# Kernel optimization log

Hardware: AMD Instinct MI355X
Metric: run time of the kernel (lower is better)

The kernel has to match this reference:

```python
import jax, jax.numpy as jnp
import numpy as np

B, S, HID, NH = 4, 2048, 1024, 16
DH = HID // NH  # 64
SCALE = 1.0 / float(np.sqrt(DH))


def _linear_params(key, scale=0.02):
    kw, kb = jax.random.split(key)
    W = jax.random.normal(kw, (HID, HID), dtype=jnp.float32) * scale
    b = jax.random.normal(kb, (HID,), dtype=jnp.float32) * scale
    return W, b


def setup_inputs() -> dict:
    key = jax.random.key(0)
    ks = jax.random.split(key, 9)
    x = jax.random.normal(ks[0], (B, S, HID), dtype=jnp.float32)
    reasoning_mask = jax.random.uniform(ks[1], (B, S, 1, 1), dtype=jnp.float32)
    Wq, bq = _linear_params(ks[2])
    Wk, bk = _linear_params(ks[3])
    Wv, bv = _linear_params(ks[4])
    Wqr, bqr = _linear_params(ks[5])
    Wkr, bkr = _linear_params(ks[6])
    Wo, bo = _linear_params(ks[7])
    return {"x": x, "reasoning_mask": reasoning_mask,
            "Wq": Wq, "bq": bq, "Wk": Wk, "bk": bk, "Wv": Wv, "bv": bv,
            "Wqr": Wqr, "bqr": bqr, "Wkr": Wkr, "bkr": bkr, "Wo": Wo, "bo": bo}


def reference(x, reasoning_mask, Wq, bq, Wk, bk, Wv, bv, Wqr, bqr, Wkr, bkr, Wo, bo):
    # Projections: x @ W + b, then view (B, S, NH, DH)
    def proj(W, b):
        return (jnp.einsum('bsh,hd->bsd', x, W) + b).reshape(B, S, NH, DH)

    q = proj(Wq, bq)
    k = proj(Wk, bk)
    v = proj(Wv, bv)
    q_r = proj(Wqr, bqr)
    k_r = proj(Wkr, bkr)

    # Reasoning-gated blend of standard and reasoning projections
    q = q * (1.0 - reasoning_mask) + q_r * reasoning_mask
    k = k * (1.0 - reasoning_mask) + k_r * reasoning_mask

    # Faithful to source: matmul over the LAST two dims of (B,S,NH,DH),
    # i.e. per-token attention ACROSS HEADS -> scores shape (B,S,NH,NH)
    scores = jnp.einsum('bshd,bsed->bshe', q, k) * SCALE
    attn = jax.nn.softmax(scores, axis=-1)  # dropout is identity at eval
    out = jnp.einsum('bshe,bsed->bshd', attn, v)  # (B,S,NH,DH)

    # Faithful transpose(1,2) + contiguous view to (B, S, HID)
    out = jnp.transpose(out, (0, 2, 1, 3)).reshape(B, -1, HID)
    return jnp.einsum('bsh,hd->bsd', out, Wo) + bo
```

## Files before the change

### kernel.cpp

```cpp
#include <hip/hip_runtime.h>
#include <hip/hip_bf16.h>


typedef __attribute__((ext_vector_type(8))) short short8;
typedef __attribute__((ext_vector_type(4))) short short4v;
typedef __attribute__((ext_vector_type(4))) float f32x4;

#define HID 1024
#define NTOK 8192
#define WT_ELEMS (1024 * 1024)

__device__ __forceinline__ short f2bs(float f) {
  __hip_bfloat16 h = __float2bfloat16(f);
  return *reinterpret_cast<short*>(&h);
}
__device__ __forceinline__ float bs2f(short s) {
  __hip_bfloat16 h;
  *reinterpret_cast<short*>(&h) = s;
  return __bfloat162float(h);
}
__device__ __forceinline__ void gload16(const void* g, void* l) {
  __builtin_amdgcn_global_load_lds(
      (const __attribute__((address_space(1))) void*)g,
      (__attribute__((address_space(3))) void*)l, 16, 0, 0);
}

#define BAR() asm volatile("s_barrier" ::: "memory")
#define VMWAIT(N) asm volatile("s_waitcnt vmcnt(" #N ")" ::: "memory")
#define SCB __builtin_amdgcn_sched_barrier(0)
#define PRIO1 __builtin_amdgcn_s_setprio(1)
#define PRIO0 __builtin_amdgcn_s_setprio(0)
#define MFMA16x16 __builtin_amdgcn_mfma_f32_16x16x32_bf16

__global__ __launch_bounds__(256) void prep_kernel(
    const float* __restrict__ W0, const float* __restrict__ W1,
    const float* __restrict__ W2, const float* __restrict__ W3,
    const float* __restrict__ W4, const float* __restrict__ W5,
    const float* __restrict__ X, short* __restrict__ WT, short* __restrict__ XB)
{
  __shared__ short sT[64][68];
  const int bid = blockIdx.x, tid = threadIdx.x;
  if (bid < 1536) {
    const int z = bid >> 8, rem = bid & 255;
    const float* W = z == 0 ? W0 : z == 1 ? W1 : z == 2 ? W2 : z == 3 ? W3
                   : z == 4 ? W4 : W5;
    short* OUT = WT + (size_t)z * WT_ELEMS;
    const int k0 = (rem & 15) * 64, n0 = (rem >> 4) * 64;
    #pragma unroll
    for (int i = 0; i < 4; i++) {
      const int li = tid + i * 256;
      const int kr = li >> 4, c4 = (li & 15) << 2;
      const f32x4 wv = *reinterpret_cast<const f32x4*>(&W[(size_t)(k0 + kr) * HID + n0 + c4]);
      short4v s4;
      #pragma unroll
      for (int j = 0; j < 4; j++) s4[j] = f2bs(wv[j]);
      *reinterpret_cast<short4v*>(&sT[kr][c4]) = s4;
    }
    __syncthreads();
    #pragma unroll
    for (int i = 0; i < 4; i++) {
      const int li = tid + i * 256;
      const int nr = li >> 4, k4 = (li & 15) << 2;
      short4v o;
      #pragma unroll
      for (int j = 0; j < 4; j++) o[j] = sT[k4 + j][nr];
      const int kcol = (k0 + k4) ^ ((nr & 7) << 3);
      *reinterpret_cast<short4v*>(&OUT[(size_t)(n0 + nr) * HID + kcol]) = o;
    }
  } else {
    const int gid = (bid - 1536) * 256 + tid;
    const int row = gid >> 7, kc = (gid & 127) << 3;
    const f32x4 a = *reinterpret_cast<const f32x4*>(&X[(size_t)row * HID + kc]);
    const f32x4 b = *reinterpret_cast<const f32x4*>(&X[(size_t)row * HID + kc + 4]);
    short8 s;
    #pragma unroll
    for (int j = 0; j < 4; j++) { s[j] = f2bs(a[j]); s[4 + j] = f2bs(b[j]); }
    const int phys = (kc & ~63) | ((kc & 63) ^ ((row & 7) << 3));
    *reinterpret_cast<short8*>(&XB[(size_t)row * HID + phys]) = s;
  }
}

__global__ __launch_bounds__(512, 2) void gated8_kernel(
    const short* __restrict__ XB, const short* __restrict__ WTbase,
    const float* __restrict__ bq, const float* __restrict__ bqr,
    const float* __restrict__ bk, const float* __restrict__ bkr,
    const float* __restrict__ MASK,
    __hip_bfloat16* __restrict__ qg, __hip_bfloat16* __restrict__ kg)
{
  __shared__ short lA[2][256][64];
  __shared__ short lB1[2][128][64];
  __shared__ short lB2[2][128][64];

  const int d = blockIdx.x;
  const int bx = d & 31, byz = d >> 5;
  const int by = byz & 7, z = byz >> 3;

  const short* W1T = WTbase + (size_t)(2 * z) * WT_ELEMS;
  const short* W2T = W1T + WT_ELEMS;
  const float* B1b = z ? bk : bq;
  const float* B2b = z ? bkr : bqr;
  __hip_bfloat16* OUT = z ? kg : qg;

  const int m0 = bx * 256, n0 = by * 128;
  const int tid = threadIdx.x, lane = tid & 63, w = tid >> 6;
  const int wr = (w >> 1) * 64, wc = (w & 1) * 64;
  const int lrow = lane & 15, lkhi = (lane >> 4) << 3;
  const int swz = (lrow & 7) << 3;
  const int srow = lane >> 3, scol = (lane & 7) << 3;

  f32x4 acc1[4][4] = {}, acc2[4][4] = {};
  short8 bf1k[4], bf2k[4], bf1b[4];
  short8 afA0, afA1, afA2, afA3;
  short8 afB0, afB1, afB2, afB3;

  auto stA2 = [&](int slot, int kt, int i0) {
    const int k0 = kt * 64;
    #pragma unroll
    for (int i = 0; i < 2; i++) {
      const int chunk = w * 4 + i0 + i;
      gload16(&XB[(size_t)(m0 + chunk * 8 + srow) * HID + k0 + scol],
              &lA[slot][chunk * 8][0]);
    }
  };
  auto stB1s = [&](int slot, int kt) {
    const int k0 = kt * 64;
    #pragma unroll
    for (int i = 0; i < 2; i++) {
      const int chunk = w * 2 + i;
      gload16(&W1T[(size_t)(n0 + chunk * 8 + srow) * HID + k0 + scol],
              &lB1[slot][chunk * 8][0]);
    }
  };
  auto stB2s = [&](int slot, int kt) {
    const int k0 = kt * 64;
    #pragma unroll
    for (int i = 0; i < 2; i++) {
      const int chunk = w * 2 + i;
      gload16(&W2T[(size_t)(n0 + chunk * 8 + srow) * HID + k0 + scol],
              &lB2[slot][chunk * 8][0]);
    }
  };
  auto rdA = [&](int s, int m, int kk) -> short8 {
    const int lk = (kk * 32 + lkhi) ^ swz;
    return *reinterpret_cast<const short8*>(&lA[s][wr + m * 16 + lrow][lk]);
  };

#define RDB1(DST, S, KK)                                                              \
  _Pragma("unroll")                                                                   \
  for (int n = 0; n < 4; n++) {                                                       \
    const int lk = ((KK) * 32 + lkhi) ^ swz;                                          \
    DST[n] = *reinterpret_cast<const short8*>(&lB1[S][wc + n * 16 + lrow][lk]);       \
  }
#define RDB2(DST, S, KK)                                                              \
  _Pragma("unroll")                                                                   \
  for (int n = 0; n < 4; n++) {                                                       \
    const int lk = ((KK) * 32 + lkhi) ^ swz;                                          \
    DST[n] = *reinterpret_cast<const short8*>(&lB2[S][wc + n * 16 + lrow][lk]);       \
  }
#define MMC1(A0, A1, A2, A3, BF)                                          \
  _Pragma("unroll")                                                       \
  for (int n = 0; n < 4; n++) {                                           \
    acc1[0][n] = MFMA16x16(A0, BF[n], acc1[0][n], 0, 0, 0);               \
    acc1[1][n] = MFMA16x16(A1, BF[n], acc1[1][n], 0, 0, 0);               \
    acc1[2][n] = MFMA16x16(A2, BF[n], acc1[2][n], 0, 0, 0);               \
    acc1[3][n] = MFMA16x16(A3, BF[n], acc1[3][n], 0, 0, 0);               \
  }
#define MMC2(A0, A1, A2, A3, BF)                                          \
  _Pragma("unroll")                                                       \
  for (int n = 0; n < 4; n++) {                                           \
    acc2[0][n] = MFMA16x16(A0, BF[n], acc2[0][n], 0, 0, 0);               \
    acc2[1][n] = MFMA16x16(A1, BF[n], acc2[1][n], 0, 0, 0);               \
    acc2[2][n] = MFMA16x16(A2, BF[n], acc2[2][n], 0, 0, 0);               \
    acc2[3][n] = MFMA16x16(A3, BF[n], acc2[3][n], 0, 0, 0);               \
  }
#define GTILE(S, SN, TS)                                                 \
  afA0 = rdA(S, 0, 0); afA1 = rdA(S, 1, 0);                              \
  afA2 = rdA(S, 2, 0); afA3 = rdA(S, 3, 0);                              \
  RDB1(bf1k, S, 0);                                                      \
  RDB2(bf2k, S, 0);                                                      \
  afB0 = rdA(S, 0, 1); afB1 = rdA(S, 1, 1);                              \
  afB2 = rdA(S, 2, 1); afB3 = rdA(S, 3, 1);                              \
  RDB1(bf1b, S, 1);                                                      \
  stA2(SN, TS, 0); stA2(SN, TS, 2); stB1s(SN, TS); stB2s(SN, TS);        \
  SCB;                                                                   \
  PRIO1; MMC1(afA0, afA1, afA2, afA3, bf1k) PRIO0;                       \
  PRIO1; MMC2(afA0, afA1, afA2, afA3, bf2k) PRIO0;                       \
  RDB2(bf2k, S, 1);                                                      \
  PRIO1; MMC1(afB0, afB1, afB2, afB3, bf1b) PRIO0;                       \
  PRIO1; MMC2(afB0, afB1, afB2, afB3, bf2k) PRIO0;                       \
  VMWAIT(0);                                                             \
  BAR();

  stA2(0, 0, 0); stA2(0, 0, 2); stB1s(0, 0); stB2s(0, 0);
  VMWAIT(0);
  BAR();

  #pragma unroll 1
  for (int i = 0; i < 16; i++) {
    const int S = i & 1, SN = S ^ 1;
    const int TS = (i < 15) ? i + 1 : 15;
    GTILE(S, SN, TS)
  }
  VMWAIT(0);
#undef GTILE
#undef MMC1
#undef MMC2
#undef RDB1
#undef RDB2

  #pragma unroll
  for (int m = 0; m < 4; m++) {
    const int rbase = m0 + wr + m * 16 + ((lane >> 4) << 2);
    #pragma unroll
    for (int n = 0; n < 4; n++) {
      const int col = n0 + wc + n * 16 + lrow;
      const float bias1 = B1b[col];
      const float bias2 = B2b[col];
      #pragma unroll
      for (int r = 0; r < 4; r++) {
        const int row = rbase + r;
        const float mk = MASK[row];
        const float val = (acc1[m][n][r] + bias1) * (1.f - mk) +
                          (acc2[m][n][r] + bias2) * mk;
        OUT[(size_t)row * HID + col] = __float2bfloat16(val);
      }
    }
  }
}

template<bool OUTF32>
__global__ __launch_bounds__(512, 2) void plain8_kernel(
    const short* __restrict__ A, const short* __restrict__ WT,
    const float* __restrict__ BIAS, void* __restrict__ OUTv)
{
  __shared__ short lA[3][256][64];
  __shared__ short lB[3][128][64];

  const int d = blockIdx.x;
  const int bx = d & 31, by = d >> 5;

  const int m0 = bx * 256, n0 = by * 128;
  const int tid = threadIdx.x, lane = tid & 63, w = tid >> 6;
  const int wr = (w >> 1) * 64, wc = (w & 1) * 64;
  const int lrow = lane & 15, lkhi = (lane >> 4) << 3;
  const int swz = (lrow & 7) << 3;
  const int srow = lane >> 3, scol = (lane & 7) << 3;

  f32x4 acc[4][4] = {};
  short8 paf[2][4], pbf[2][4];

  auto stTrip = [&](int slot, int kt, int t) {
    const int k0 = kt * 64;
    if (t == 0) {
      #pragma unroll
      for (int i = 0; i < 3; i++) {
        const int chunk = w * 4 + i;
        gload16(&A[(size_t)(m0 + chunk * 8 + srow) * HID + k0 + scol],
                &lA[slot][chunk * 8][0]);
      }
    } else {
      const int chunk = w * 4 + 3;
      gload16(&A[(size_t)(m0 + chunk * 8 + srow) * HID + k0 + scol],
              &lA[slot][chunk * 8][0]);
      #pragma unroll
      for (int i = 0; i < 2; i++) {
        const int bchunk = w * 2 + i;
        gload16(&WT[(size_t)(n0 + bchunk * 8 + srow) * HID + k0 + scol],
                &lB[slot][bchunk * 8][0]);
      }
    }
  };

#define RDP(S, KK)                                                                    \
  _Pragma("unroll")                                                                   \
  for (int m = 0; m < 4; m++) {                                                       \
    const int lk = ((KK) * 32 + lkhi) ^ swz;                                          \
    paf[KK][m] = *reinterpret_cast<const short8*>(&lA[S][wr + m * 16 + lrow][lk]);    \
    pbf[KK][m] = *reinterpret_cast<const short8*>(&lB[S][wc + m * 16 + lrow][lk]);    \
  }
#define PMM16(KK)                                                                     \
  _Pragma("unroll")                                                                   \
  for (int m = 0; m < 4; m++)                                                         \
    _Pragma("unroll")                                                                 \
    for (int n = 0; n < 4; n++)                                                       \
      acc[m][n] = MFMA16x16(paf[KK][m], pbf[KK][n], acc[m][n], 0, 0, 0);

  stTrip(0, 0, 0); stTrip(0, 0, 1);
  stTrip(1, 1, 0); stTrip(1, 1, 1);
  VMWAIT(6);
  BAR();

  int s = 0, s2 = 2;
  #pragma unroll 1
  for (int t = 0; t < 16; t++) {
    const int TS = (t < 14) ? t + 2 : 15;
    RDP(s, 0)
    RDP(s, 1)
    stTrip(s2, TS, 0); stTrip(s2, TS, 1);
    SCB;
    PRIO1; PMM16(0) PRIO0;
    PRIO1; PMM16(1) PRIO0;
    VMWAIT(6);
    BAR();
    s = (s == 2) ? 0 : s + 1;
    s2 = (s2 == 2) ? 0 : s2 + 1;
  }
  VMWAIT(0);
#undef PMM16
#undef RDP

  #pragma unroll
  for (int m = 0; m < 4; m++) {
    const int rbase = m0 + wr + m * 16 + ((lane >> 4) << 2);
    #pragma unroll
    for (int n = 0; n < 4; n++) {
      const int col = n0 + wc + n * 16 + lrow;
      const float bias = BIAS[col];
      #pragma unroll
      for (int r = 0; r < 4; r++) {
        const float val = acc[m][n][r] + bias;
        const size_t oidx = (size_t)(rbase + r) * HID + col;
        if (OUTF32) ((float*)OUTv)[oidx] = val;
        else ((__hip_bfloat16*)OUTv)[oidx] = __float2bfloat16(val);
      }
    }
  }
}

__global__ __launch_bounds__(256) void attn_kernel(
    const __hip_bfloat16* __restrict__ Q, const __hip_bfloat16* __restrict__ K,
    const __hip_bfloat16* __restrict__ V, __hip_bfloat16* __restrict__ O)
{
  const int t = blockIdx.x;
  const int b = t >> 11, s = t & 2047;
  __shared__ float sQ[16][68], sK[16][68], sV[16][68];
  __shared__ float sA[16][17];
  const int tid = threadIdx.x;
  const size_t tb = (size_t)t * HID;

  {
    const int h = tid >> 4, d0 = (tid & 15) << 2;
    const int o = (h << 6) + d0;
    const short4v qv = *reinterpret_cast<const short4v*>(&((const short*)Q)[tb + o]);
    const short4v kv = *reinterpret_cast<const short4v*>(&((const short*)K)[tb + o]);
    const short4v vv = *reinterpret_cast<const short4v*>(&((const short*)V)[tb + o]);
    #pragma unroll
    for (int j = 0; j < 4; j++) {
      sQ[h][d0 + j] = bs2f(qv[j]);
      sK[h][d0 + j] = bs2f(kv[j]);
      sV[h][d0 + j] = bs2f(vv[j]);
    }
  }
  __syncthreads();

  const int h = tid >> 4, e = tid & 15;
  float sc = 0.f;
  #pragma unroll
  for (int dd = 0; dd < 64; dd++) sc += sQ[h][dd] * sK[e][dd];
  sc *= 0.125f;

  float mx = sc;
  mx = fmaxf(mx, __shfl_xor(mx, 1));
  mx = fmaxf(mx, __shfl_xor(mx, 2));
  mx = fmaxf(mx, __shfl_xor(mx, 4));
  mx = fmaxf(mx, __shfl_xor(mx, 8));
  const float p = __expf(sc - mx);
  float sm = p;
  sm += __shfl_xor(sm, 1);
  sm += __shfl_xor(sm, 2);
  sm += __shfl_xor(sm, 4);
  sm += __shfl_xor(sm, 8);
  sA[h][e] = p / sm;
  __syncthreads();

  const int row7 = (s >> 4) & 7;
  const size_t ob = ((size_t)b * 2048 + (s >> 4)) * HID + ((size_t)(s & 15) << 6);
  {
    const int hh = tid >> 4, d4 = (tid & 15) << 2;
    f32x4 o = {0.f, 0.f, 0.f, 0.f};
    #pragma unroll
    for (int e2 = 0; e2 < 16; e2++) {
      const float a = sA[hh][e2];
      #pragma unroll
      for (int j = 0; j < 4; j++) o[j] += a * sV[e2][d4 + j];
    }
    short4v ov;
    #pragma unroll
    for (int j = 0; j < 4; j++) ov[j] = f2bs(o[j]);
    *reinterpret_cast<short4v*>(
        &((short*)O)[ob + (size_t)hh * 128 * HID + (d4 ^ (row7 << 3))]) = ov;
  }
}

extern "C" void kernel_launch(void* const* d_in, const int* in_sizes, int n_in,
                              void* d_out, int out_size, void* d_ws, size_t ws_size,
                              hipStream_t stream) {
  (void)in_sizes; (void)n_in; (void)out_size; (void)ws_size;
  const float* x   = (const float*)d_in[0];
  const float* rm  = (const float*)d_in[1];
  const float* Wq  = (const float*)d_in[2];
  const float* bq  = (const float*)d_in[3];
  const float* Wk  = (const float*)d_in[4];
  const float* bk  = (const float*)d_in[5];
  const float* Wv  = (const float*)d_in[6];
  const float* bv  = (const float*)d_in[7];
  const float* Wqr = (const float*)d_in[8];
  const float* bqr = (const float*)d_in[9];
  const float* Wkr = (const float*)d_in[10];
  const float* bkr = (const float*)d_in[11];
  const float* Wo  = (const float*)d_in[12];
  const float* bo  = (const float*)d_in[13];

  char* ws = (char*)d_ws;
  short* wt = (short*)ws;
  __hip_bfloat16* qg = (__hip_bfloat16*)(ws + 12u * 1024 * 1024);
  __hip_bfloat16* vv = (__hip_bfloat16*)(ws + 28u * 1024 * 1024);
  __hip_bfloat16* ar = (__hip_bfloat16*)(ws + 44u * 1024 * 1024);
  short* xb = (short*)d_out;
  __hip_bfloat16* kg = (__hip_bfloat16*)((char*)d_out + 16u * 1024 * 1024);

  prep_kernel<<<dim3(5632), 256, 0, stream>>>(Wq, Wqr, Wk, Wkr, Wv, Wo, x, wt, xb);
  gated8_kernel<<<dim3(512), 512, 0, stream>>>(xb, wt, bq, bqr, bk, bkr, rm, qg, kg);
  plain8_kernel<false><<<dim3(256), 512, 0, stream>>>(xb, wt + (size_t)4 * WT_ELEMS, bv, vv);
  attn_kernel<<<dim3(NTOK), 256, 0, stream>>>(qg, kg, vv, ar);
  plain8_kernel<true><<<dim3(256), 512, 0, stream>>>((const short*)ar,
                                                     wt + (size_t)5 * WT_ELEMS, bo, d_out);
}
```

Measured before the change: 146.9 us.

## Compute per-token head attention with MFMA, one wavefront per token

Rewrites the cross-head attention kernel so each wavefront handles one token and uses 16x16 bf16 MFMA for both the QK^T scores and the PV product, instead of a 256-thread block per token doing scalar FP32 dot products out of shared memory. Softmax is done on the MFMA accumulator layout with lane shuffles, and probabilities are staged through a small per-wave LDS tile. The launch shrinks to a quarter of the blocks. The risks are that V is gathered with strided scalar loads and the output is written as scalar bf16 stores, which may be poorly coalesced.

```diff
diff --git a/kernel.cpp b/kernel.cpp
--- a/kernel.cpp
+++ b/kernel.cpp
@@ -331,64 +331,70 @@
     const __hip_bfloat16* __restrict__ Q, const __hip_bfloat16* __restrict__ K,
     const __hip_bfloat16* __restrict__ V, __hip_bfloat16* __restrict__ O)
 {
-  const int t = blockIdx.x;
+  __shared__ short sP[4][16][32];
+  const int tid = threadIdx.x, w = tid >> 6, lane = tid & 63;
+  const int t = blockIdx.x * 4 + w;
   const int b = t >> 11, s = t & 2047;
-  __shared__ float sQ[16][68], sK[16][68], sV[16][68];
-  __shared__ float sA[16][17];
-  const int tid = threadIdx.x;
   const size_t tb = (size_t)t * HID;
-
-  {
-    const int h = tid >> 4, d0 = (tid & 15) << 2;
-    const int o = (h << 6) + d0;
-    const short4v qv = *reinterpret_cast<const short4v*>(&((const short*)Q)[tb + o]);
-    const short4v kv = *reinterpret_cast<const short4v*>(&((const short*)K)[tb + o]);
-    const short4v vv = *reinterpret_cast<const short4v*>(&((const short*)V)[tb + o]);
-    #pragma unroll
-    for (int j = 0; j < 4; j++) {
-      sQ[h][d0 + j] = bs2f(qv[j]);
-      sK[h][d0 + j] = bs2f(kv[j]);
-      sV[h][d0 + j] = bs2f(vv[j]);
-    }
-  }
-  __syncthreads();
-
-  const int h = tid >> 4, e = tid & 15;
-  float sc = 0.f;
-  #pragma unroll
-  for (int dd = 0; dd < 64; dd++) sc += sQ[h][dd] * sK[e][dd];
-  sc *= 0.125f;
-
-  float mx = sc;
-  mx = fmaxf(mx, __shfl_xor(mx, 1));
-  mx = fmaxf(mx, __shfl_xor(mx, 2));
-  mx = fmaxf(mx, __shfl_xor(mx, 4));
-  mx = fmaxf(mx, __shfl_xor(mx, 8));
-  const float p = __expf(sc - mx);
-  float sm = p;
-  sm += __shfl_xor(sm, 1);
-  sm += __shfl_xor(sm, 2);
-  sm += __shfl_xor(sm, 4);
-  sm += __shfl_xor(sm, 8);
-  sA[h][e] = p / sm;
-  __syncthreads();
-
+  const short* q = (const short*)Q;
+  const short* k = (const short*)K;
+  const short* v = (const short*)V;
+  const int lrow = lane & 15, lk = lane >> 4;
+
+  *reinterpret_cast<short8*>(&sP[w][lrow][lk * 8]) = short8{0,0,0,0,0,0,0,0};
+
+  f32x4 sc4 = {0.f, 0.f, 0.f, 0.f};
+  #pragma unroll
+  for (int kk = 0; kk < 2; kk++) {
+    const size_t off = tb + (size_t)lrow * 64 + kk * 32 + lk * 8;
+    const short8 qf = *reinterpret_cast<const short8*>(&q[off]);
+    const short8 kf = *reinterpret_cast<const short8*>(&k[off]);
+    sc4 = MFMA16x16(qf, kf, sc4, 0, 0, 0);
+  }
+
+  float p[4];
+  #pragma unroll
+  for (int r = 0; r < 4; r++) {
+    const float x = sc4[r] * 0.125f;
+    float mx = x;
+    mx = fmaxf(mx, __shfl_xor(mx, 1));
+    mx = fmaxf(mx, __shfl_xor(mx, 2));
+    mx = fmaxf(mx, __shfl_xor(mx, 4));
+    mx = fmaxf(mx, __shfl_xor(mx, 8));
+    const float e = __expf(x - mx);
+    float sm = e;
+    sm += __shfl_xor(sm, 1);
+    sm += __shfl_xor(sm, 2);
+    sm += __shfl_xor(sm, 4);
+    sm += __shfl_xor(sm, 8);
+    p[r] = e / sm;
+  }
+
+  #pragma unroll
+  for (int r = 0; r < 4; r++)
+    sP[w][lk * 4 + r][lrow] = f2bs(p[r]);
+  asm volatile("s_waitcnt lgkmcnt(0)" ::: "memory");
+  SCB;
+
+  const short8 af = *reinterpret_cast<const short8*>(&sP[w][lrow][lk * 8]);
   const int row7 = (s >> 4) & 7;
-  const size_t ob = ((size_t)b * 2048 + (s >> 4)) * HID + ((size_t)(s & 15) << 6);
-  {
-    const int hh = tid >> 4, d4 = (tid & 15) << 2;
+  const size_t obase = ((size_t)b * 2048 + (s >> 4)) * HID + ((size_t)(s & 15) << 6);
+  #pragma unroll
+  for (int db = 0; db < 4; db++) {
+    short8 bf = {0, 0, 0, 0, 0, 0, 0, 0};
+    if (lane < 32) {
+      #pragma unroll
+      for (int j = 0; j < 8; j++)
+        bf[j] = v[tb + (size_t)(lk * 8 + j) * 64 + db * 16 + lrow];
+    }
     f32x4 o = {0.f, 0.f, 0.f, 0.f};
-    #pragma unroll
-    for (int e2 = 0; e2 < 16; e2++) {
-      const float a = sA[hh][e2];
-      #pragma unroll
-      for (int j = 0; j < 4; j++) o[j] += a * sV[e2][d4 + j];
-    }
-    short4v ov;
-    #pragma unroll
-    for (int j = 0; j < 4; j++) ov[j] = f2bs(o[j]);
-    *reinterpret_cast<short4v*>(
-        &((short*)O)[ob + (size_t)hh * 128 * HID + (d4 ^ (row7 << 3))]) = ov;
+    o = MFMA16x16(af, bf, o, 0, 0, 0);
+    #pragma unroll
+    for (int r = 0; r < 4; r++) {
+      const int h = lk * 4 + r;
+      const int dd = db * 16 + lrow;
+      O[obase + (size_t)h * 128 * HID + (dd ^ (row7 << 3))] = __float2bfloat16(o[r]);
+    }
   }
 }
 
@@ -422,7 +428,7 @@
   prep_kernel<<<dim3(5632), 256, 0, stream>>>(Wq, Wqr, Wk, Wkr, Wv, Wo, x, wt, xb);
   gated8_kernel<<<dim3(512), 512, 0, stream>>>(xb, wt, bq, bqr, bk, bkr, rm, qg, kg);
   plain8_kernel<false><<<dim3(256), 512, 0, stream>>>(xb, wt + (size_t)4 * WT_ELEMS, bv, vv);
-  attn_kernel<<<dim3(NTOK), 256, 0, stream>>>(qg, kg, vv, ar);
+  attn_kernel<<<dim3(NTOK / 4), 256, 0, stream>>>(qg, kg, vv, ar);
   plain8_kernel<true><<<dim3(256), 512, 0, stream>>>((const short*)ar,
                                                      wt + (size_t)5 * WT_ELEMS, bo, d_out);
 }
```

New measurement: 137.8 us. 1.07x faster.
